# Performance work log

Measured on AMD Instinct MI355X. Metric: run time of the kernel, lower is better.

## Reference

```python
import jax, jax.numpy as jnp
import numpy as np

N = 50000   # nodes
E = 800000  # edges (avg degree 16)
D = 64      # indim == outdim
H = 64      # hiddim


def setup_inputs() -> dict:
    key = jax.random.key(0)
    ks = jax.random.split(key, 11)

    def w(k, shape):
        return (jax.random.normal(k, shape, jnp.float32) / jnp.sqrt(shape[0])).astype(jnp.float32)

    return {
        "h": jax.random.normal(ks[0], (N, D), jnp.float32),
        "e": jax.random.normal(ks[1], (E, D), jnp.float32),
        "src": jax.random.randint(ks[2], (E,), 0, N, jnp.int32),
        "dst": jax.random.randint(ks[3], (E,), 0, N, jnp.int32),
        # linear_h MLP (bias=False): D -> H -> D
        "Wh1": w(ks[4], (D, H)), "Wh2": w(ks[5], (H, D)),
        # linear_e MLP (bias=False): D -> H -> D
        "We1": w(ks[6], (D, H)), "We2": w(ks[7], (H, D)),
        # proj MLP (bias=True): 3D -> H -> D
        "Wp1": w(ks[8], (3 * D, H)), "bp1": jnp.zeros((H,), jnp.float32),
        "Wp2": w(ks[9], (H, D)), "bp2": jnp.zeros((D,), jnp.float32),
        # attn_linear (bias=False): 3D -> 1
        "Wa": w(ks[10], (3 * D, 1)),
    }


def reference(h, e, src, dst, Wh1, Wh2, We1, We2, Wp1, bp1, Wp2, bp2, Wa):
    relu = jax.nn.relu
    # node / edge feature MLPs (Linear -> ReLU -> Linear, no bias)
    z_h = relu(h @ Wh1) @ Wh2            # [N, D]
    z_e = relu(e @ We1) @ We2            # [E, D]
    # per-edge concat [z_e, z_src, z_dst]
    z = jnp.concatenate([z_e, z_h[src], z_h[dst]], axis=1)  # [E, 3D]
    # edge projection MLP (with bias)
    e_proj = relu(z @ Wp1 + bp1) @ Wp2 + bp2                 # [E, D]
    # attention score + attn activation (ReLU)
    a = relu((z @ Wa)[:, 0])                                  # [E]
    # segment softmax over incoming edges of each destination node
    m = jax.ops.segment_max(a, dst, num_segments=N)
    m = jnp.where(jnp.isfinite(m), m, 0.0)                    # zero-degree nodes
    ex = jnp.exp(a - m[dst])
    s = jax.ops.segment_sum(ex, dst, num_segments=N)
    alpha = ex / jnp.maximum(s[dst], 1e-9)                    # [E]
    # weighted scatter-sum of source features
    h_out = jax.ops.segment_sum(alpha[:, None] * z_h[src], dst, num_segments=N)  # [N, D]
    # final activation (batch_norm=False, dropout=0)
    return relu(h_out), relu(e_proj)
```

## Files before the change

### kernel.cpp

```cpp
#include <hip/hip_runtime.h>
#include <hip/hip_bf16.h>

#define DIM 64
#define BM 128

typedef __attribute__((ext_vector_type(8))) short bf16x8;
typedef __attribute__((ext_vector_type(4))) float f32x4;

__device__ __forceinline__ short f2bf_hw(float x) {
    __hip_bfloat16 b = __float2bfloat16(x);
    return (short)reinterpret_cast<unsigned short&>(b);
}
__device__ __forceinline__ float bf2f_hw(short s) {
    unsigned u = ((unsigned)(unsigned short)s) << 16;
    return __uint_as_float(u);
}
__device__ __forceinline__ void split8(float4 a, float4 b, bf16x8& hi, bf16x8& lo) {
    float v[8] = {a.x, a.y, a.z, a.w, b.x, b.y, b.z, b.w};
    #pragma unroll
    for (int i = 0; i < 8; ++i) {
        short h = f2bf_hw(v[i]);
        hi[i] = h;
        lo[i] = f2bf_hw(v[i] - bf2f_hw(h));
    }
}
__device__ __forceinline__ int swz(int row, int colbyte) {
    return row * 256 + (colbyte ^ ((row & 7) << 4));
}

__global__ __launch_bounds__(256) void k_prep(
    const float* __restrict__ We1, const float* __restrict__ We2,
    const float* __restrict__ Wp1, const float* __restrict__ Wp2,
    const float* __restrict__ Wh1, const float* __restrict__ Wh2,
    unsigned short* __restrict__ whi, unsigned short* __restrict__ wlo)
{
    int t = blockIdx.x * 256 + threadIdx.x;
    int e_ = t & 7, lane = (t >> 3) & 63, frag = (t >> 9) & 7, layer = t >> 12;
    int kt = frag >> 2, nt = frag & 3;
    int k = kt * 32 + ((lane >> 4) * 8) + e_;
    int n = nt * 16 + (lane & 15);
    const float* W;
    switch (layer) {
        case 0: W = We1; break;
        case 1: W = We2; break;
        case 2: W = Wp1; break;
        case 3: W = Wp2; break;
        case 4: W = Wh1; break;
        case 5: W = Wh2; break;
        case 6: W = Wp1 + 64 * 64; break;
        default: W = Wp1 + 128 * 64; break;
    }
    float w = W[k * 64 + n];
    short h = f2bf_hw(w);
    whi[t] = (unsigned short)h;
    wlo[t] = (unsigned short)f2bf_hw(w - bf2f_hw(h));
}

__global__ __launch_bounds__(256) void node_mfma(
    const float* __restrict__ h,
    const unsigned short* __restrict__ whi, const unsigned short* __restrict__ wlo,
    const float* __restrict__ Wa,
    float* __restrict__ z_h, float* __restrict__ u_s, float* __restrict__ u_d,
    float* __restrict__ as_, float* __restrict__ ad_, int N)
{
    __shared__ float act[BM * 64];
    char* lds = (char*)act;
    const int lane  = threadIdx.x & 63;
    const int wave  = threadIdx.x >> 6;
    const int wrow0 = wave * 32;
    const long node0 = (long)blockIdx.x * BM;
    const int g   = lane >> 4;
    const int c15 = lane & 15;

    float was[4], wad[4];
    #pragma unroll
    for (int nt = 0; nt < 4; ++nt) {
        was[nt] = Wa[64  + nt * 16 + c15];
        wad[nt] = Wa[128 + nt * 16 + c15];
    }

    f32x4 acc[2][4];
    auto zacc = [&]() {
        #pragma unroll
        for (int mt = 0; mt < 2; ++mt)
            #pragma unroll
            for (int nt = 0; nt < 4; ++nt)
                #pragma unroll
                for (int rr = 0; rr < 4; ++rr) acc[mt][nt][rr] = 0.f;
    };

    auto mfma_layer = [&](int layer) {
        #pragma unroll
        for (int kt = 0; kt < 2; ++kt) {
            bf16x8 ah[2], al[2];
            #pragma unroll
            for (int mt = 0; mt < 2; ++mt) {
                float4 a0, a1;
                if (layer == 4) {
                    long nr = node0 + wrow0 + mt * 16 + c15; if (nr >= N) nr = N - 1;
                    const float* p = h + nr * 64 + kt * 32 + g * 8;
                    a0 = *(const float4*)p;
                    a1 = *(const float4*)(p + 4);
                } else {
                    int row = wrow0 + mt * 16 + c15;
                    int cb  = kt * 128 + g * 32;
                    a0 = *(const float4*)(lds + swz(row, cb));
                    a1 = *(const float4*)(lds + swz(row, cb + 16));
                }
                split8(a0, a1, ah[mt], al[mt]);
            }
            #pragma unroll
            for (int nt = 0; nt < 4; ++nt) {
                int fo = ((layer * 8 + kt * 4 + nt) * 64 + lane) * 8;
                bf16x8 bh = *(const bf16x8*)(whi + fo);
                bf16x8 bl = *(const bf16x8*)(wlo + fo);
                #pragma unroll
                for (int mt = 0; mt < 2; ++mt) {
                    acc[mt][nt] = __builtin_amdgcn_mfma_f32_16x16x32_bf16(ah[mt], bh, acc[mt][nt], 0, 0, 0);
                    acc[mt][nt] = __builtin_amdgcn_mfma_f32_16x16x32_bf16(ah[mt], bl, acc[mt][nt], 0, 0, 0);
                    acc[mt][nt] = __builtin_amdgcn_mfma_f32_16x16x32_bf16(al[mt], bh, acc[mt][nt], 0, 0, 0);
                }
            }
        }
    };

    auto writeback = [&](bool relu) {
        #pragma unroll
        for (int mt = 0; mt < 2; ++mt)
            #pragma unroll
            for (int nt = 0; nt < 4; ++nt)
                #pragma unroll
                for (int rr = 0; rr < 4; ++rr) {
                    int row  = wrow0 + mt * 16 + g * 4 + rr;
                    int colb = (nt * 16 + c15) * 4;
                    float v = acc[mt][nt][rr];
                    if (relu) v = fmaxf(v, 0.f);
                    *(float*)(lds + swz(row, colb)) = v;
                }
    };

    auto store_global = [&](float* __restrict__ out) {
        #pragma unroll
        for (int mt = 0; mt < 2; ++mt)
            #pragma unroll
            for (int nt = 0; nt < 4; ++nt)
                #pragma unroll
                for (int rr = 0; rr < 4; ++rr) {
                    long nr = node0 + wrow0 + mt * 16 + g * 4 + rr; if (nr >= N) nr = N - 1;
                    out[nr * 64 + nt * 16 + c15] = acc[mt][nt][rr];
                }
    };

    zacc(); mfma_layer(4); writeback(true);
    zacc(); mfma_layer(5);

    #pragma unroll
    for (int mt = 0; mt < 2; ++mt) {
        float ps[4], pd[4];
        #pragma unroll
        for (int rr = 0; rr < 4; ++rr) {
            ps[rr] = acc[mt][0][rr] * was[0] + acc[mt][1][rr] * was[1]
                   + acc[mt][2][rr] * was[2] + acc[mt][3][rr] * was[3];
            pd[rr] = acc[mt][0][rr] * wad[0] + acc[mt][1][rr] * wad[1]
                   + acc[mt][2][rr] * wad[2] + acc[mt][3][rr] * wad[3];
        }
        #pragma unroll
        for (int off = 1; off < 16; off <<= 1)
            #pragma unroll
            for (int rr = 0; rr < 4; ++rr) {
                ps[rr] += __shfl_xor(ps[rr], off);
                pd[rr] += __shfl_xor(pd[rr], off);
            }
        if (c15 == 0) {
            #pragma unroll
            for (int rr = 0; rr < 4; ++rr) {
                long nr = node0 + wrow0 + mt * 16 + g * 4 + rr; if (nr >= N) nr = N - 1;
                as_[nr] = ps[rr];
                ad_[nr] = pd[rr];
            }
        }
    }
    store_global(z_h);
    writeback(false);

    zacc(); mfma_layer(6); store_global(u_s);
    zacc(); mfma_layer(7); store_global(u_d);
}

__global__ __launch_bounds__(256) void edge_mfma(
    const float* __restrict__ e, const int* __restrict__ src, const int* __restrict__ dst,
    const float* __restrict__ u_s, const float* __restrict__ u_d,
    const float* __restrict__ as_, const float* __restrict__ ad_,
    const unsigned short* __restrict__ whi, const unsigned short* __restrict__ wlo,
    const float* __restrict__ Wa, const float* __restrict__ bp1, const float* __restrict__ bp2,
    float* __restrict__ eproj, float* __restrict__ abuf,
    int* __restrict__ cursor, int* __restrict__ eidx, int E)
{
    __shared__ float act[BM * 64];
    char* lds = (char*)act;
    const int lane  = threadIdx.x & 63;
    const int wave  = threadIdx.x >> 6;
    const int wrow0 = wave * 32;
    const long edge0 = (long)blockIdx.x * BM;
    const int g   = lane >> 4;
    const int c15 = lane & 15;

    int sn[2][4], dn[2][4];
    #pragma unroll
    for (int mt = 0; mt < 2; ++mt)
        #pragma unroll
        for (int rr = 0; rr < 4; ++rr) {
            long er0 = edge0 + wrow0 + mt * 16 + g * 4 + rr;
            long er = er0 >= E ? E - 1 : er0;
            sn[mt][rr] = src[er]; dn[mt][rr] = dst[er];
            if (c15 == 0 && er0 < E) {
                int p = atomicAdd(&cursor[dn[mt][rr]], 1);
                eidx[p] = (int)er0;
            }
        }

    float waf[4], b1f[4], b2f[4];
    #pragma unroll
    for (int nt = 0; nt < 4; ++nt) {
        waf[nt] = Wa[nt * 16 + c15];
        b1f[nt] = bp1[nt * 16 + c15];
        b2f[nt] = bp2[nt * 16 + c15];
    }

    float uv[2][4][4], asv[2][4];
    #pragma unroll
    for (int mt = 0; mt < 2; ++mt)
        #pragma unroll
        for (int rr = 0; rr < 4; ++rr) {
            const float* us = u_s + (size_t)sn[mt][rr] * DIM;
            const float* ud = u_d + (size_t)dn[mt][rr] * DIM;
            #pragma unroll
            for (int nt = 0; nt < 4; ++nt)
                uv[mt][nt][rr] = us[nt * 16 + c15] + ud[nt * 16 + c15] + b1f[nt];
            asv[mt][rr] = as_[sn[mt][rr]] + ad_[dn[mt][rr]];
        }

    f32x4 acc[2][4];
    auto zacc = [&]() {
        #pragma unroll
        for (int mt = 0; mt < 2; ++mt)
            #pragma unroll
            for (int nt = 0; nt < 4; ++nt)
                #pragma unroll
                for (int rr = 0; rr < 4; ++rr) acc[mt][nt][rr] = 0.f;
    };

    auto mfma_layer = [&](int layer) {
        #pragma unroll
        for (int kt = 0; kt < 2; ++kt) {
            bf16x8 ah[2], al[2];
            #pragma unroll
            for (int mt = 0; mt < 2; ++mt) {
                float4 a0, a1;
                if (layer == 0) {
                    long er = edge0 + wrow0 + mt * 16 + c15; if (er >= E) er = E - 1;
                    const float* p = e + er * 64 + kt * 32 + g * 8;
                    a0 = *(const float4*)p;
                    a1 = *(const float4*)(p + 4);
                } else {
                    int row = wrow0 + mt * 16 + c15;
                    int cb  = kt * 128 + g * 32;
                    a0 = *(const float4*)(lds + swz(row, cb));
                    a1 = *(const float4*)(lds + swz(row, cb + 16));
                }
                split8(a0, a1, ah[mt], al[mt]);
            }
            #pragma unroll
            for (int nt = 0; nt < 4; ++nt) {
                int fo = ((layer * 8 + kt * 4 + nt) * 64 + lane) * 8;
                bf16x8 bh = *(const bf16x8*)(whi + fo);
                bf16x8 bl = *(const bf16x8*)(wlo + fo);
                #pragma unroll
                for (int mt = 0; mt < 2; ++mt) {
                    acc[mt][nt] = __builtin_amdgcn_mfma_f32_16x16x32_bf16(ah[mt], bh, acc[mt][nt], 0, 0, 0);
                    acc[mt][nt] = __builtin_amdgcn_mfma_f32_16x16x32_bf16(ah[mt], bl, acc[mt][nt], 0, 0, 0);
                    acc[mt][nt] = __builtin_amdgcn_mfma_f32_16x16x32_bf16(al[mt], bh, acc[mt][nt], 0, 0, 0);
                }
            }
        }
    };

    auto writeback = [&](bool relu) {
        #pragma unroll
        for (int mt = 0; mt < 2; ++mt)
            #pragma unroll
            for (int nt = 0; nt < 4; ++nt)
                #pragma unroll
                for (int rr = 0; rr < 4; ++rr) {
                    int row  = wrow0 + mt * 16 + g * 4 + rr;
                    int colb = (nt * 16 + c15) * 4;
                    float v = acc[mt][nt][rr];
                    if (relu) v = fmaxf(v, 0.f);
                    *(float*)(lds + swz(row, colb)) = v;
                }
    };

    zacc(); mfma_layer(0); writeback(true);
    zacc(); mfma_layer(1);

    #pragma unroll
    for (int mt = 0; mt < 2; ++mt) {
        float part[4];
        #pragma unroll
        for (int rr = 0; rr < 4; ++rr)
            part[rr] = acc[mt][0][rr] * waf[0] + acc[mt][1][rr] * waf[1]
                     + acc[mt][2][rr] * waf[2] + acc[mt][3][rr] * waf[3];
        #pragma unroll
        for (int off = 1; off < 16; off <<= 1)
            #pragma unroll
            for (int rr = 0; rr < 4; ++rr) part[rr] += __shfl_xor(part[rr], off);
        if (c15 == 0) {
            #pragma unroll
            for (int rr = 0; rr < 4; ++rr) {
                long er = edge0 + wrow0 + mt * 16 + g * 4 + rr; if (er >= E) er = E - 1;
                abuf[er] = fmaxf(part[rr] + asv[mt][rr], 0.f);
            }
        }
    }
    writeback(false);

    zacc(); mfma_layer(2);
    #pragma unroll
    for (int mt = 0; mt < 2; ++mt)
        #pragma unroll
        for (int nt = 0; nt < 4; ++nt)
            #pragma unroll
            for (int rr = 0; rr < 4; ++rr)
                acc[mt][nt][rr] += uv[mt][nt][rr];
    writeback(true);

    zacc(); mfma_layer(3);
    #pragma unroll
    for (int mt = 0; mt < 2; ++mt)
        #pragma unroll
        for (int nt = 0; nt < 4; ++nt)
            #pragma unroll
            for (int rr = 0; rr < 4; ++rr) {
                long er = edge0 + wrow0 + mt * 16 + g * 4 + rr; if (er >= E) er = E - 1;
                eproj[er * 64 + nt * 16 + c15] = fmaxf(acc[mt][nt][rr] + b2f[nt], 0.f);
            }
}

__global__ __launch_bounds__(256) void k_hist(
    const int* __restrict__ dst, int* __restrict__ cnt, int E)
{
    int i = blockIdx.x * 256 + threadIdx.x;
    if (i < E) atomicAdd(&cnt[dst[i]], 1);
}

__global__ __launch_bounds__(256) void k_scan1(
    const int* __restrict__ cnt, int* __restrict__ ofs, int* __restrict__ bsum, int N)
{
    __shared__ int sm[256];
    int t = threadIdx.x, i = blockIdx.x * 256 + t;
    int v = (i < N) ? cnt[i] : 0;
    sm[t] = v;
    __syncthreads();
    #pragma unroll
    for (int off = 1; off < 256; off <<= 1) {
        int tmp = (t >= off) ? sm[t - off] : 0;
        __syncthreads();
        sm[t] += tmp;
        __syncthreads();
    }
    if (i < N) ofs[i] = sm[t] - v;
    if (t == 255) bsum[blockIdx.x] = sm[255];
}

__global__ __launch_bounds__(256) void k_scan2(int* __restrict__ bsum, int NB)
{
    __shared__ int sm[256];
    int t = threadIdx.x;
    int v = (t < NB) ? bsum[t] : 0;
    sm[t] = v;
    __syncthreads();
    #pragma unroll
    for (int off = 1; off < 256; off <<= 1) {
        int tmp = (t >= off) ? sm[t - off] : 0;
        __syncthreads();
        sm[t] += tmp;
        __syncthreads();
    }
    if (t < NB) bsum[t] = sm[t] - v;
}

__global__ __launch_bounds__(256) void k_scan3(
    int* __restrict__ ofs, int* __restrict__ cursor,
    const int* __restrict__ bsum, int N)
{
    int i = blockIdx.x * 256 + threadIdx.x;
    if (i < N) {
        int o = ofs[i] + bsum[blockIdx.x];
        ofs[i] = o;
        cursor[i] = o;
    }
}

__global__ __launch_bounds__(256) void k_aggregate(
    const float* __restrict__ abuf, const int* __restrict__ eidx,
    const int* __restrict__ ofs, const int* __restrict__ cnt,
    const int* __restrict__ src, const float* __restrict__ z_h,
    float* __restrict__ hout, int N)
{
    int wid  = (blockIdx.x * 256 + threadIdx.x) >> 6;
    int lane = threadIdx.x & 63;
    if (wid >= N) return;
    int grp = lane >> 4, c15 = lane & 15;

    int begin = ofs[wid];
    int deg   = cnt[wid];

    float4 acc = make_float4(0.f, 0.f, 0.f, 0.f);
    float inv_s;

    if (deg <= 64) {
        float a = 0.f; int sidx = 0;
        if (lane < deg) {
            int eid = eidx[begin + lane];
            a    = abuf[eid];
            sidx = src[eid];
        }
        float m = a;
        #pragma unroll
        for (int off = 32; off; off >>= 1) m = fmaxf(m, __shfl_xor(m, off));

        float ex = (lane < deg) ? __expf(a - m) : 0.f;
        float s = ex;
        #pragma unroll
        for (int off = 32; off; off >>= 1) s += __shfl_xor(s, off);
        inv_s = 1.0f / fmaxf(s, 1e-9f);

        int trips = (deg + 3) >> 2;
        for (int i = 0; i < trips; ++i) {
            int k = grp + 4 * i;
            float w  = __shfl(ex,   k & 63);
            int   sk = __shfl(sidx, k & 63);
            if (k < deg) {
                const float4 v = *(const float4*)(z_h + (size_t)sk * DIM + c15 * 4);
                acc.x = fmaf(w, v.x, acc.x);
                acc.y = fmaf(w, v.y, acc.y);
                acc.z = fmaf(w, v.z, acc.z);
                acc.w = fmaf(w, v.w, acc.w);
            }
        }
    } else {
        float m = 0.f;
        for (int k = lane; k < deg; k += 64) m = fmaxf(m, abuf[eidx[begin + k]]);
        #pragma unroll
        for (int off = 32; off; off >>= 1) m = fmaxf(m, __shfl_xor(m, off));

        float s = 0.f;
        for (int k = lane; k < deg; k += 64) s += __expf(abuf[eidx[begin + k]] - m);
        #pragma unroll
        for (int off = 32; off; off >>= 1) s += __shfl_xor(s, off);
        inv_s = 1.0f / fmaxf(s, 1e-9f);

        for (int k = grp; k < deg; k += 4) {
            int eid = eidx[begin + k];
            float w = __expf(abuf[eid] - m);
            const float4 v = *(const float4*)(z_h + (size_t)src[eid] * DIM + c15 * 4);
            acc.x = fmaf(w, v.x, acc.x);
            acc.y = fmaf(w, v.y, acc.y);
            acc.z = fmaf(w, v.z, acc.z);
            acc.w = fmaf(w, v.w, acc.w);
        }
    }

    #pragma unroll
    for (int off = 16; off <= 32; off <<= 1) {
        acc.x += __shfl_xor(acc.x, off);
        acc.y += __shfl_xor(acc.y, off);
        acc.z += __shfl_xor(acc.z, off);
        acc.w += __shfl_xor(acc.w, off);
    }
    if (grp == 0) {
        float4 r = make_float4(fmaxf(acc.x * inv_s, 0.f), fmaxf(acc.y * inv_s, 0.f),
                               fmaxf(acc.z * inv_s, 0.f), fmaxf(acc.w * inv_s, 0.f));
        *(float4*)(hout + (size_t)wid * DIM + c15 * 4) = r;
    }
}

extern "C" void kernel_launch(void* const* d_in, const int* in_sizes, int n_in,
                              void* d_out, int out_size, void* d_ws, size_t ws_size,
                              hipStream_t stream)
{
    const float* h   = (const float*)d_in[0];
    const float* e   = (const float*)d_in[1];
    const int*   src = (const int*)d_in[2];
    const int*   dst = (const int*)d_in[3];
    const float* Wh1 = (const float*)d_in[4];
    const float* Wh2 = (const float*)d_in[5];
    const float* We1 = (const float*)d_in[6];
    const float* We2 = (const float*)d_in[7];
    const float* Wp1 = (const float*)d_in[8];
    const float* bp1 = (const float*)d_in[9];
    const float* Wp2 = (const float*)d_in[10];
    const float* bp2 = (const float*)d_in[11];
    const float* Wa  = (const float*)d_in[12];

    const int N = in_sizes[0] / DIM;
    const int E = in_sizes[1] / DIM;

    float* ws   = (float*)d_ws;
    float* z_h  = ws;  ws += (size_t)N * DIM;
    float* u_s  = ws;  ws += (size_t)N * DIM;
    float* u_d  = ws;  ws += (size_t)N * DIM;
    float* as_  = ws;  ws += N;
    float* ad_  = ws;  ws += N;
    float* abuf = ws;  ws += E;
    int* cnt    = (int*)ws;  ws += N;
    int* ofs    = (int*)ws;  ws += N;
    int* cursor = (int*)ws;  ws += N;
    int* eidx   = (int*)ws;  ws += E;
    int* bsum   = (int*)ws;  ws += 256;
    unsigned short* whi = (unsigned short*)ws;  ws += 32768 / 2;
    unsigned short* wlo = (unsigned short*)ws;  ws += 32768 / 2;

    float* hout  = (float*)d_out;
    float* eproj = hout + (size_t)N * DIM;

    const int NB = (N + 255) / 256;

    hipMemsetAsync(cnt, 0, (size_t)N * sizeof(int), stream);

    k_prep<<<128, 256, 0, stream>>>(We1, We2, Wp1, Wp2, Wh1, Wh2, whi, wlo);

    k_hist<<<(E + 255) / 256, 256, 0, stream>>>(dst, cnt, E);
    k_scan1<<<NB, 256, 0, stream>>>(cnt, ofs, bsum, N);
    k_scan2<<<1, 256, 0, stream>>>(bsum, NB);
    k_scan3<<<NB, 256, 0, stream>>>(ofs, cursor, bsum, N);

    node_mfma<<<(N + BM - 1) / BM, 256, 0, stream>>>(
        h, whi, wlo, Wa, z_h, u_s, u_d, as_, ad_, N);

    edge_mfma<<<(E + BM - 1) / BM, 256, 0, stream>>>(
        e, src, dst, u_s, u_d, as_, ad_, whi, wlo, Wa, bp1, bp2,
        eproj, abuf, cursor, eidx, E);

    k_aggregate<<<((N * 64) + 255) / 256, 256, 0, stream>>>(
        abuf, eidx, ofs, cnt, src, z_h, hout, N);
}
```

Measured before the change: 380.3 us.

## Move CSR fill out of edge kernel, add nontemporal streaming and MFMA priority

Moves the atomic cursor fill that builds the per-destination edge index into its own small kernel, so edge_mfma no longer performs scattered atomics. Streaming loads of e and stores of eproj and abuf become nontemporal so they do not pollute the cache. s_setprio is raised around the MFMA blocks to favour matrix issue across waves. The cost is one extra kernel launch and a second pass over dst.

```diff
diff --git a/kernel.cpp b/kernel.cpp
--- a/kernel.cpp
+++ b/kernel.cpp
@@ -15,8 +15,8 @@
     unsigned u = ((unsigned)(unsigned short)s) << 16;
     return __uint_as_float(u);
 }
-__device__ __forceinline__ void split8(float4 a, float4 b, bf16x8& hi, bf16x8& lo) {
-    float v[8] = {a.x, a.y, a.z, a.w, b.x, b.y, b.z, b.w};
+__device__ __forceinline__ void split8(f32x4 a, f32x4 b, bf16x8& hi, bf16x8& lo) {
+    float v[8] = {a[0], a[1], a[2], a[3], b[0], b[1], b[2], b[3]};
     #pragma unroll
     for (int i = 0; i < 8; ++i) {
         short h = f2bf_hw(v[i]);
@@ -95,20 +95,21 @@
             bf16x8 ah[2], al[2];
             #pragma unroll
             for (int mt = 0; mt < 2; ++mt) {
-                float4 a0, a1;
+                f32x4 a0, a1;
                 if (layer == 4) {
                     long nr = node0 + wrow0 + mt * 16 + c15; if (nr >= N) nr = N - 1;
-                    const float* p = h + nr * 64 + kt * 32 + g * 8;
-                    a0 = *(const float4*)p;
-                    a1 = *(const float4*)(p + 4);
+                    const f32x4* p = (const f32x4*)(h + nr * 64 + kt * 32 + g * 8);
+                    a0 = p[0];
+                    a1 = p[1];
                 } else {
                     int row = wrow0 + mt * 16 + c15;
                     int cb  = kt * 128 + g * 32;
-                    a0 = *(const float4*)(lds + swz(row, cb));
-                    a1 = *(const float4*)(lds + swz(row, cb + 16));
+                    a0 = *(const f32x4*)(lds + swz(row, cb));
+                    a1 = *(const f32x4*)(lds + swz(row, cb + 16));
                 }
                 split8(a0, a1, ah[mt], al[mt]);
             }
+            __builtin_amdgcn_s_setprio(1);
             #pragma unroll
             for (int nt = 0; nt < 4; ++nt) {
                 int fo = ((layer * 8 + kt * 4 + nt) * 64 + lane) * 8;
@@ -121,6 +122,7 @@
                     acc[mt][nt] = __builtin_amdgcn_mfma_f32_16x16x32_bf16(al[mt], bh, acc[mt][nt], 0, 0, 0);
                 }
             }
+            __builtin_amdgcn_s_setprio(0);
         }
     };
 
@@ -193,8 +195,7 @@
     const float* __restrict__ as_, const float* __restrict__ ad_,
     const unsigned short* __restrict__ whi, const unsigned short* __restrict__ wlo,
     const float* __restrict__ Wa, const float* __restrict__ bp1, const float* __restrict__ bp2,
-    float* __restrict__ eproj, float* __restrict__ abuf,
-    int* __restrict__ cursor, int* __restrict__ eidx, int E)
+    float* __restrict__ eproj, float* __restrict__ abuf, int E)
 {
     __shared__ float act[BM * 64];
     char* lds = (char*)act;
@@ -210,13 +211,8 @@
     for (int mt = 0; mt < 2; ++mt)
         #pragma unroll
         for (int rr = 0; rr < 4; ++rr) {
-            long er0 = edge0 + wrow0 + mt * 16 + g * 4 + rr;
-            long er = er0 >= E ? E - 1 : er0;
+            long er = edge0 + wrow0 + mt * 16 + g * 4 + rr; if (er >= E) er = E - 1;
             sn[mt][rr] = src[er]; dn[mt][rr] = dst[er];
-            if (c15 == 0 && er0 < E) {
-                int p = atomicAdd(&cursor[dn[mt][rr]], 1);
-                eidx[p] = (int)er0;
-            }
         }
 
     float waf[4], b1f[4], b2f[4];
@@ -256,20 +252,21 @@
             bf16x8 ah[2], al[2];
             #pragma unroll
             for (int mt = 0; mt < 2; ++mt) {
-                float4 a0, a1;
+                f32x4 a0, a1;
                 if (layer == 0) {
                     long er = edge0 + wrow0 + mt * 16 + c15; if (er >= E) er = E - 1;
-                    const float* p = e + er * 64 + kt * 32 + g * 8;
-                    a0 = *(const float4*)p;
-                    a1 = *(const float4*)(p + 4);
+                    const f32x4* p = (const f32x4*)(e + er * 64 + kt * 32 + g * 8);
+                    a0 = __builtin_nontemporal_load(p);
+                    a1 = __builtin_nontemporal_load(p + 1);
                 } else {
                     int row = wrow0 + mt * 16 + c15;
                     int cb  = kt * 128 + g * 32;
-                    a0 = *(const float4*)(lds + swz(row, cb));
-                    a1 = *(const float4*)(lds + swz(row, cb + 16));
+                    a0 = *(const f32x4*)(lds + swz(row, cb));
+                    a1 = *(const f32x4*)(lds + swz(row, cb + 16));
                 }
                 split8(a0, a1, ah[mt], al[mt]);
             }
+            __builtin_amdgcn_s_setprio(1);
             #pragma unroll
             for (int nt = 0; nt < 4; ++nt) {
                 int fo = ((layer * 8 + kt * 4 + nt) * 64 + lane) * 8;
@@ -282,6 +279,7 @@
                     acc[mt][nt] = __builtin_amdgcn_mfma_f32_16x16x32_bf16(al[mt], bh, acc[mt][nt], 0, 0, 0);
                 }
             }
+            __builtin_amdgcn_s_setprio(0);
         }
     };
 
@@ -318,7 +316,7 @@
             #pragma unroll
             for (int rr = 0; rr < 4; ++rr) {
                 long er = edge0 + wrow0 + mt * 16 + g * 4 + rr; if (er >= E) er = E - 1;
-                abuf[er] = fmaxf(part[rr] + asv[mt][rr], 0.f);
+                __builtin_nontemporal_store(fmaxf(part[rr] + asv[mt][rr], 0.f), abuf + er);
             }
         }
     }
@@ -342,7 +340,8 @@
             #pragma unroll
             for (int rr = 0; rr < 4; ++rr) {
                 long er = edge0 + wrow0 + mt * 16 + g * 4 + rr; if (er >= E) er = E - 1;
-                eproj[er * 64 + nt * 16 + c15] = fmaxf(acc[mt][nt][rr] + b2f[nt], 0.f);
+                __builtin_nontemporal_store(fmaxf(acc[mt][nt][rr] + b2f[nt], 0.f),
+                                            eproj + er * 64 + nt * 16 + c15);
             }
 }
 
@@ -398,6 +397,16 @@
         int o = ofs[i] + bsum[blockIdx.x];
         ofs[i] = o;
         cursor[i] = o;
+    }
+}
+
+__global__ __launch_bounds__(256) void k_fill(
+    const int* __restrict__ dst, int* __restrict__ cursor, int* __restrict__ eidx, int E)
+{
+    int i = blockIdx.x * 256 + threadIdx.x;
+    if (i < E) {
+        int p = atomicAdd(&cursor[dst[i]], 1);
+        eidx[p] = i;
     }
 }
 
@@ -534,13 +543,14 @@
     k_scan1<<<NB, 256, 0, stream>>>(cnt, ofs, bsum, N);
     k_scan2<<<1, 256, 0, stream>>>(bsum, NB);
     k_scan3<<<NB, 256, 0, stream>>>(ofs, cursor, bsum, N);
+    k_fill<<<(E + 255) / 256, 256, 0, stream>>>(dst, cursor, eidx, E);
 
     node_mfma<<<(N + BM - 1) / BM, 256, 0, stream>>>(
         h, whi, wlo, Wa, z_h, u_s, u_d, as_, ad_, N);
 
     edge_mfma<<<(E + BM - 1) / BM, 256, 0, stream>>>(
         e, src, dst, u_s, u_d, as_, ad_, whi, wlo, Wa, bp1, bp2,
-        eproj, abuf, cursor, eidx, E);
+        eproj, abuf, E);
 
     k_aggregate<<<((N * 64) + 255) / 256, 256, 0, stream>>>(
         abuf, eidx, ofs, cnt, src, z_h, hout, N);
```

New measurement: 347.7 us. 1.09x faster.
